# Performance work log

Measured on AMD Instinct MI355X. Metric: run time of the kernel, lower is better.

The kernel has to match this reference:

```python
import jax, jax.numpy as jnp
import numpy as np

N_HEAD = 16
N_KV_HEAD = 4
HEAD_DIM = 128
ROPE_BASE = 10000.0


def _rope_cos_sin(T, offset, dtype):
    # inv_freq: [head_dim//2]
    inv_freq = 1.0 / (ROPE_BASE ** (jnp.arange(0, HEAD_DIM, 2, dtype=jnp.float32) / HEAD_DIM))
    pos = jnp.arange(offset, offset + T, dtype=jnp.float32)
    ang = pos[:, None] * inv_freq[None, :]              # [T, hd/2]
    emb = jnp.concatenate([ang, ang], axis=-1)           # [T, hd]
    return jnp.cos(emb).astype(dtype), jnp.sin(emb).astype(dtype)


def _rotate_half(t):
    half = t.shape[-1] // 2
    return jnp.concatenate([-t[..., half:], t[..., :half]], axis=-1)


def _apply_rope(t, cos, sin):
    # t: [B, h, T, hd]; cos/sin: [T, hd]
    return t * cos[None, None] + _rotate_half(t) * sin[None, None]


def setup_inputs() -> dict:
    key = jax.random.key(0)
    ks = jax.random.split(key, 5)
    B, T, C = 4, 2048, 2048
    scale = 0.02
    return {
        "x": jax.random.normal(ks[0], (B, T, C), dtype=jnp.float32),
        "Wq": jax.random.normal(ks[1], (C, C), dtype=jnp.float32) * scale,
        "Wk": jax.random.normal(ks[2], (N_KV_HEAD * HEAD_DIM, C), dtype=jnp.float32) * scale,
        "Wv": jax.random.normal(ks[3], (N_KV_HEAD * HEAD_DIM, C), dtype=jnp.float32) * scale,
        "Wo": jax.random.normal(ks[4], (C, C), dtype=jnp.float32) * scale,
        "offset": 0,
    }


def reference(x, Wq, Wk, Wv, Wo, offset):
    B, T, C = x.shape
    n_rep = N_HEAD // N_KV_HEAD
    # projections (torch Linear: x @ W.T)
    q = (x @ Wq.T).reshape(B, T, N_HEAD, HEAD_DIM).transpose(0, 2, 1, 3)     # [B,H,T,d]
    k = (x @ Wk.T).reshape(B, T, N_KV_HEAD, HEAD_DIM).transpose(0, 2, 1, 3)  # [B,G,T,d]
    v = (x @ Wv.T).reshape(B, T, N_KV_HEAD, HEAD_DIM).transpose(0, 2, 1, 3)  # [B,G,T,d]
    cos, sin = _rope_cos_sin(T, offset, x.dtype)
    q = _apply_rope(q, cos, sin)
    k = _apply_rope(k, cos, sin)
    # GQA without materializing replicated K/V: group q heads by kv head
    qg = q.reshape(B, N_KV_HEAD, n_rep, T, HEAD_DIM)
    scale = 1.0 / jnp.sqrt(jnp.asarray(HEAD_DIM, dtype=x.dtype))
    scores = jnp.einsum('bgrtd,bgsd->bgrts', qg, k) * scale                  # [B,G,r,T,S]
    causal = jnp.tril(jnp.ones((T, T), dtype=bool))
    scores = jnp.where(causal[None, None, None], scores, jnp.asarray(-jnp.inf, dtype=scores.dtype))
    attn = jax.nn.softmax(scores, axis=-1)
    yg = jnp.einsum('bgrts,bgsd->bgrtd', attn, v)                            # [B,G,r,T,d]
    y = yg.reshape(B, N_HEAD, T, HEAD_DIM).transpose(0, 2, 1, 3).reshape(B, T, C)
    return y @ Wo.T
```

## Files before the change

### kernel.cpp

```cpp
#include <hip/hip_runtime.h>
#include <math.h>

#define BATCH 4
#define SEQ   2048
#define CDIM  2048
#define NH    16
#define NG    4
#define HD    128
#define MTOT  (BATCH*SEQ)
#define KVD   (NG*HD)

typedef __attribute__((ext_vector_type(8))) short     bf16x8;
typedef __attribute__((ext_vector_type(8))) unsigned short u16x8;
typedef __attribute__((ext_vector_type(4))) float     f32x4;
typedef unsigned short ushort_t;

static __device__ __forceinline__ unsigned short f2bf(float f) {
  unsigned u = __float_as_uint(f);
  u += 0x7FFF + ((u >> 16) & 1);
  return (unsigned short)(u >> 16);
}
static __device__ __forceinline__ float bf2f(unsigned short h) {
  return __uint_as_float(((unsigned)h) << 16);
}

#define GLOAD_LDS16(gp, lp)                                                        \
  __builtin_amdgcn_global_load_lds((const __attribute__((address_space(1))) void*)(gp), \
                                   (__attribute__((address_space(3))) void*)(lp),  \
                                   16, 0, 0)

__global__ __launch_bounds__(256) void cvt_f32_bf16(
    const float* __restrict__ s, ushort_t* __restrict__ d, int n8)
{
  int i = blockIdx.x * 256 + threadIdx.x;
  if (i >= n8) return;
  const float4* p = (const float4*)(s + (size_t)i * 8);
  float4 a = p[0], b = p[1];
  u16x8 o;
  o[0] = f2bf(a.x); o[1] = f2bf(a.y); o[2] = f2bf(a.z); o[3] = f2bf(a.w);
  o[4] = f2bf(b.x); o[5] = f2bf(b.y); o[6] = f2bf(b.z); o[7] = f2bf(b.w);
  *(u16x8*)(d + (size_t)i * 8) = o;
}

template<int OUTMODE>
__global__ __launch_bounds__(256) void gemm_bt_bf16(
    const ushort_t* __restrict__ A, const ushort_t* __restrict__ B,
    void* __restrict__ C, int M, int N, int K)
{
  __shared__ ushort_t As[128 * 32];
  __shared__ ushort_t Bs[128 * 32];
  const int tid  = threadIdx.x;
  const int lane = tid & 63, w = tid >> 6;
  const int wm = (w >> 1) * 64, wn = (w & 1) * 64;
  const int bm = blockIdx.x * 128, bn = blockIdx.y * 128;

  f32x4 acc[4][4];
#pragma unroll
  for (int m = 0; m < 4; ++m)
#pragma unroll
    for (int n = 0; n < 4; ++n) acc[m][n] = (f32x4){0.f, 0.f, 0.f, 0.f};

  const int srow = tid >> 2;
  const int scol = (tid & 3) * 8;
  const ushort_t* Ap = A + (size_t)(bm + srow) * K + scol;
  const ushort_t* Bp = B + (size_t)(bn + srow) * K + scol;

  const int fr = lane & 15, fg = lane >> 4;

  for (int k0 = 0; k0 < K; k0 += 32) {
    GLOAD_LDS16(Ap + k0,                  As + tid * 8);
    GLOAD_LDS16(Ap + (size_t)64 * K + k0, As + 2048 + tid * 8);
    GLOAD_LDS16(Bp + k0,                  Bs + tid * 8);
    GLOAD_LDS16(Bp + (size_t)64 * K + k0, Bs + 2048 + tid * 8);
    __syncthreads();

    bf16x8 av[4], bv[4];
#pragma unroll
    for (int m = 0; m < 4; ++m)
      av[m] = *(const bf16x8*)(As + (wm + m * 16 + fr) * 32 + fg * 8);
#pragma unroll
    for (int n = 0; n < 4; ++n)
      bv[n] = *(const bf16x8*)(Bs + (wn + n * 16 + fr) * 32 + fg * 8);
#pragma unroll
    for (int m = 0; m < 4; ++m)
#pragma unroll
      for (int n = 0; n < 4; ++n)
        acc[m][n] = __builtin_amdgcn_mfma_f32_16x16x32_bf16(av[m], bv[n], acc[m][n], 0, 0, 0);
    __syncthreads();
  }

  if constexpr (OUTMODE == 2) {
    __shared__ ushort_t Ct[128 * 144];
#pragma unroll
    for (int m = 0; m < 4; ++m)
#pragma unroll
      for (int n = 0; n < 4; ++n)
#pragma unroll
        for (int r = 0; r < 4; ++r)
          Ct[(wn + n * 16 + fr) * 144 + wm + m * 16 + fg * 4 + r] = f2bf(acc[m][n][r]);
    __syncthreads();
    const int col_l = tid >> 1, part = tid & 1;
    ushort_t* dst = (ushort_t*)C + (size_t)(bn + col_l) * M + bm + part * 64;
#pragma unroll
    for (int j = 0; j < 8; ++j)
      *(bf16x8*)(dst + j * 8) = *(const bf16x8*)(Ct + col_l * 144 + part * 64 + j * 8);
  } else {
#pragma unroll
    for (int m = 0; m < 4; ++m)
#pragma unroll
      for (int n = 0; n < 4; ++n)
#pragma unroll
        for (int r = 0; r < 4; ++r) {
          const int row = bm + wm + m * 16 + fg * 4 + r;
          const int col = bn + wn + n * 16 + fr;
          if (OUTMODE == 1) ((float*)C)[(size_t)row * N + col] = acc[m][n][r];
          else              ((ushort_t*)C)[(size_t)row * N + col] = f2bf(acc[m][n][r]);
        }
  }
}

__global__ __launch_bounds__(256) void rope_bf16(
    ushort_t* __restrict__ qf, ushort_t* __restrict__ kf, const int* __restrict__ off)
{
  const int idx  = blockIdx.x * 256 + threadIdx.x;
  const int qtot = MTOT * NH * (HD / 2);
  const int ktot = MTOT * NG * (HD / 2);
  if (idx >= qtot + ktot) return;

  ushort_t* buf; int row, head, i, cols;
  if (idx < qtot) {
    buf = qf; cols = NH * HD;
    row = idx / (NH * (HD / 2));
    int rem = idx % (NH * (HD / 2));
    head = rem / (HD / 2); i = rem % (HD / 2);
  } else {
    int id2 = idx - qtot;
    buf = kf; cols = NG * HD;
    row = id2 / (NG * (HD / 2));
    int rem = id2 % (NG * (HD / 2));
    head = rem / (HD / 2); i = rem % (HD / 2);
  }
  const int   t   = row % SEQ;
  const float pos = (float)(t + off[0]);
  const float inv = powf(10000.0f, -(float)i * (1.0f / 64.0f));
  const float ang = pos * inv;
  const float c = cosf(ang), s = sinf(ang);

  ushort_t* p = buf + (size_t)row * cols + head * HD + i;
  const float lo = bf2f(p[0]), hi = bf2f(p[64]);
  p[0]  = f2bf(lo * c - hi * s);
  p[64] = f2bf(hi * c + lo * s);
}

#define KPAD 136
#define VPAD 72

__global__ __launch_bounds__(256) void attn_mfma(
    const ushort_t* __restrict__ qf,
    const ushort_t* __restrict__ kf,
    const ushort_t* __restrict__ vT,
    ushort_t* __restrict__ yb)
{
  __shared__ ushort_t Ks[64 * KPAD];
  __shared__ ushort_t Vt[128 * VPAD];
  __shared__ ushort_t Ps[64 * VPAD];

  const int tid  = threadIdx.x;
  const int lane = tid & 63, wq = tid >> 6;
  const int bh = blockIdx.x, b = bh >> 4, h = bh & 15, g = h >> 2;
  const int qb = blockIdx.y * 64;
  const int fr = lane & 15, fg = lane >> 4;

  bf16x8 qv[4];
  {
    const ushort_t* qp = qf + (size_t)(b * SEQ + qb + wq * 16 + fr) * CDIM + h * HD + fg * 8;
#pragma unroll
    for (int ds = 0; ds < 4; ++ds) qv[ds] = *(const bf16x8*)(qp + ds * 32);
  }

  f32x4 o[8];
#pragma unroll
  for (int n = 0; n < 8; ++n) o[n] = (f32x4){0.f, 0.f, 0.f, 0.f};
  float mrow[4] = {-1e30f, -1e30f, -1e30f, -1e30f};
  float lrow[4] = {0.f, 0.f, 0.f, 0.f};

  const float scale = 0.088388347648318447f;
  const int nkv = qb / 64 + 1;

  const ushort_t* vtb0 = vT + (size_t)(g * HD) * MTOT + (size_t)b * SEQ;

  for (int kb = 0; kb < nkv; ++kb) {
    const int s0 = kb * 64;
    __syncthreads();

#pragma unroll
    for (int it = 0; it < 4; ++it) {
      const int f4 = tid + it * 256;
      const int r = f4 >> 4, c8 = (f4 & 15) * 8;
      bf16x8 kx = *(const bf16x8*)(kf + (size_t)(b * SEQ + s0 + r) * KVD + g * HD + c8);
      *(bf16x8*)(Ks + r * KPAD + c8) = kx;
    }
    const ushort_t* vtb = vtb0 + s0;
#pragma unroll
    for (int it = 0; it < 4; ++it) {
      const int gi = tid + it * 256;
      const int d = gi >> 3, gg = gi & 7;
      bf16x8 vx = *(const bf16x8*)(vtb + (size_t)d * MTOT + gg * 8);
      *(bf16x8*)(Vt + d * VPAD + gg * 8) = vx;
    }
    __syncthreads();

    f32x4 st[4];
#pragma unroll
    for (int n = 0; n < 4; ++n) st[n] = (f32x4){0.f, 0.f, 0.f, 0.f};
#pragma unroll
    for (int ds = 0; ds < 4; ++ds) {
#pragma unroll
      for (int n = 0; n < 4; ++n) {
        bf16x8 kv = *(const bf16x8*)(Ks + (n * 16 + fr) * KPAD + ds * 32 + fg * 8);
        st[n] = __builtin_amdgcn_mfma_f32_16x16x32_bf16(qv[ds], kv, st[n], 0, 0, 0);
      }
    }

    float es[4];
#pragma unroll
    for (int r = 0; r < 4; ++r) {
      const int grow = qb + wq * 16 + fg * 4 + r;
      float sv[4], mx = -1e30f;
#pragma unroll
      for (int n = 0; n < 4; ++n) {
        const int col = s0 + n * 16 + fr;
        float v = st[n][r] * scale;
        v = (col <= grow) ? v : -1e30f;
        sv[n] = v; mx = fmaxf(mx, v);
      }
      mx = fmaxf(mx, __shfl_xor(mx, 1, 64));
      mx = fmaxf(mx, __shfl_xor(mx, 2, 64));
      mx = fmaxf(mx, __shfl_xor(mx, 4, 64));
      mx = fmaxf(mx, __shfl_xor(mx, 8, 64));
      const float mnew = fmaxf(mrow[r], mx);
      es[r] = __expf(mrow[r] - mnew);
      float sum = 0.f;
      const int prow = (wq * 16 + fg * 4 + r) * VPAD;
#pragma unroll
      for (int n = 0; n < 4; ++n) {
        const float p = __expf(sv[n] - mnew);
        sum += p;
        Ps[prow + n * 16 + fr] = f2bf(p);
      }
      sum += __shfl_xor(sum, 1, 64);
      sum += __shfl_xor(sum, 2, 64);
      sum += __shfl_xor(sum, 4, 64);
      sum += __shfl_xor(sum, 8, 64);
      lrow[r] = lrow[r] * es[r] + sum;
      mrow[r] = mnew;
    }
#pragma unroll
    for (int n = 0; n < 8; ++n)
#pragma unroll
      for (int r = 0; r < 4; ++r) o[n][r] *= es[r];

#pragma unroll
    for (int ks = 0; ks < 2; ++ks) {
      bf16x8 pa = *(const bf16x8*)(Ps + (wq * 16 + fr) * VPAD + ks * 32 + fg * 8);
#pragma unroll
      for (int n = 0; n < 8; ++n) {
        bf16x8 vb = *(const bf16x8*)(Vt + (n * 16 + fr) * VPAD + ks * 32 + fg * 8);
        o[n] = __builtin_amdgcn_mfma_f32_16x16x32_bf16(pa, vb, o[n], 0, 0, 0);
      }
    }
  }

#pragma unroll
  for (int n = 0; n < 8; ++n)
#pragma unroll
    for (int r = 0; r < 4; ++r) {
      const int row = qb + wq * 16 + fg * 4 + r;
      const int col = h * HD + n * 16 + fr;
      yb[(size_t)(b * SEQ + row) * CDIM + col] = f2bf(o[n][r] / lrow[r]);
    }
}

extern "C" void kernel_launch(void* const* d_in, const int* in_sizes, int n_in,
                              void* d_out, int out_size, void* d_ws, size_t ws_size,
                              hipStream_t stream) {
  const float* x  = (const float*)d_in[0];
  const float* Wq = (const float*)d_in[1];
  const float* Wk = (const float*)d_in[2];
  const float* Wv = (const float*)d_in[3];
  const float* Wo = (const float*)d_in[4];
  const int*   off = (const int*)d_in[5];
  float* out = (float*)d_out;

  ushort_t* xb  = (ushort_t*)d_ws;
  ushort_t* wqb = xb  + (size_t)MTOT * CDIM;
  ushort_t* wkb = wqb + (size_t)CDIM * CDIM;
  ushort_t* wvb = wkb + (size_t)KVD * CDIM;
  ushort_t* wob = wvb + (size_t)KVD * CDIM;
  ushort_t* qb_ = wob + (size_t)CDIM * CDIM;
  ushort_t* kb_ = qb_ + (size_t)MTOT * CDIM;
  ushort_t* vT_ = kb_ + (size_t)MTOT * KVD;
  ushort_t* yb_ = vT_ + (size_t)MTOT * KVD;

  dim3 blk(256);

  int n8;
  n8 = MTOT * CDIM / 8; cvt_f32_bf16<<<(n8 + 255) / 256, blk, 0, stream>>>(x,  xb,  n8);
  n8 = CDIM * CDIM / 8; cvt_f32_bf16<<<(n8 + 255) / 256, blk, 0, stream>>>(Wq, wqb, n8);
  n8 = KVD  * CDIM / 8; cvt_f32_bf16<<<(n8 + 255) / 256, blk, 0, stream>>>(Wk, wkb, n8);
  n8 = KVD  * CDIM / 8; cvt_f32_bf16<<<(n8 + 255) / 256, blk, 0, stream>>>(Wv, wvb, n8);
  n8 = CDIM * CDIM / 8; cvt_f32_bf16<<<(n8 + 255) / 256, blk, 0, stream>>>(Wo, wob, n8);

  gemm_bt_bf16<0><<<dim3(MTOT / 128, CDIM / 128), blk, 0, stream>>>(xb, wqb, qb_, MTOT, CDIM, CDIM);
  gemm_bt_bf16<0><<<dim3(MTOT / 128, KVD / 128),  blk, 0, stream>>>(xb, wkb, kb_, MTOT, KVD, CDIM);
  gemm_bt_bf16<2><<<dim3(MTOT / 128, KVD / 128),  blk, 0, stream>>>(xb, wvb, vT_, MTOT, KVD, CDIM);

  const int total_pairs = MTOT * (NH + NG) * (HD / 2);
  rope_bf16<<<(total_pairs + 255) / 256, blk, 0, stream>>>(qb_, kb_, off);

  attn_mfma<<<dim3(BATCH * NH, SEQ / 64), blk, 0, stream>>>(qb_, kb_, vT_, yb_);

  gemm_bt_bf16<1><<<dim3(MTOT / 128, CDIM / 128), blk, 0, stream>>>(yb_, wob, out, MTOT, CDIM, CDIM);
}
```

Measured before the change: 856.5 us.

## Enlarge attention query tile to 128 rows with register-prefetched KV pipeline

The attention kernel now processes 128 query rows per block, with each wave owning two 16-row MFMA tiles, so every K/V tile staged in shared memory is reused across twice as many queries. The next K/V tile is prefetched into registers during compute and written to LDS after a barrier. The change also skips fully masked tiles per wave, drops mask work on fully unmasked tiles, folds the softmax scale into an exp2 constant, and adds s_setprio around the MFMA sections. The cost is more register pressure (launch bounds now request 2 blocks per SM), half as many blocks in the grid, and an extra barrier per iteration.

After: 720.2 us. 1.19x faster.

```diff
diff --git a/kernel.cpp b/kernel.cpp
--- a/kernel.cpp
+++ b/kernel.cpp
@@ -155,7 +155,7 @@
 #define KPAD 136
 #define VPAD 72
 
-__global__ __launch_bounds__(256) void attn_mfma(
+__global__ __launch_bounds__(256, 2) void attn_mfma(
     const ushort_t* __restrict__ qf,
     const ushort_t* __restrict__ kf,
     const ushort_t* __restrict__ vT,
@@ -163,122 +163,168 @@
 {
   __shared__ ushort_t Ks[64 * KPAD];
   __shared__ ushort_t Vt[128 * VPAD];
-  __shared__ ushort_t Ps[64 * VPAD];
+  __shared__ ushort_t Ps[128 * VPAD];
 
   const int tid  = threadIdx.x;
   const int lane = tid & 63, wq = tid >> 6;
   const int bh = blockIdx.x, b = bh >> 4, h = bh & 15, g = h >> 2;
-  const int qb = blockIdx.y * 64;
+  const int qb = blockIdx.y * 128;
   const int fr = lane & 15, fg = lane >> 4;
-
-  bf16x8 qv[4];
-  {
-    const ushort_t* qp = qf + (size_t)(b * SEQ + qb + wq * 16 + fr) * CDIM + h * HD + fg * 8;
-#pragma unroll
-    for (int ds = 0; ds < 4; ++ds) qv[ds] = *(const bf16x8*)(qp + ds * 32);
-  }
-
-  f32x4 o[8];
-#pragma unroll
-  for (int n = 0; n < 8; ++n) o[n] = (f32x4){0.f, 0.f, 0.f, 0.f};
-  float mrow[4] = {-1e30f, -1e30f, -1e30f, -1e30f};
-  float lrow[4] = {0.f, 0.f, 0.f, 0.f};
-
-  const float scale = 0.088388347648318447f;
-  const int nkv = qb / 64 + 1;
+  const int wrow0 = qb + wq * 32;
+
+  bf16x8 qv[2][4];
+#pragma unroll
+  for (int rb = 0; rb < 2; ++rb) {
+    const ushort_t* qp = qf + (size_t)(b * SEQ + wrow0 + rb * 16 + fr) * CDIM + h * HD + fg * 8;
+#pragma unroll
+    for (int ds = 0; ds < 4; ++ds) qv[rb][ds] = *(const bf16x8*)(qp + ds * 32);
+  }
+
+  f32x4 o[2][8];
+#pragma unroll
+  for (int rb = 0; rb < 2; ++rb)
+#pragma unroll
+    for (int n = 0; n < 8; ++n) o[rb][n] = (f32x4){0.f, 0.f, 0.f, 0.f};
+  float mrow[2][4], lrow[2][4];
+#pragma unroll
+  for (int rb = 0; rb < 2; ++rb)
+#pragma unroll
+    for (int r = 0; r < 4; ++r) { mrow[rb][r] = -1e30f; lrow[rb][r] = 0.f; }
+
+  const float K2 = 0.12751743671f;
+  const int nkv = qb / 64 + 2;
 
   const ushort_t* vtb0 = vT + (size_t)(g * HD) * MTOT + (size_t)b * SEQ;
+  const ushort_t* kfb  = kf + (size_t)(b * SEQ) * KVD + g * HD;
+
+  bf16x8 kpre[4], vpre[4];
+
+  auto prefetch = [&](int s0n) {
+#pragma unroll
+    for (int it = 0; it < 4; ++it) {
+      const int f4 = tid + it * 256;
+      kpre[it] = *(const bf16x8*)(kfb + (size_t)(s0n + (f4 >> 4)) * KVD + (f4 & 15) * 8);
+    }
+#pragma unroll
+    for (int it = 0; it < 4; ++it) {
+      const int f4 = tid + it * 256;
+      vpre[it] = *(const bf16x8*)(vtb0 + s0n + (size_t)(f4 >> 3) * MTOT + (f4 & 7) * 8);
+    }
+  };
+  auto writetile = [&]() {
+#pragma unroll
+    for (int it = 0; it < 4; ++it) {
+      const int f4 = tid + it * 256;
+      *(bf16x8*)(Ks + (f4 >> 4) * KPAD + (f4 & 15) * 8) = kpre[it];
+    }
+#pragma unroll
+    for (int it = 0; it < 4; ++it) {
+      const int f4 = tid + it * 256;
+      *(bf16x8*)(Vt + (f4 >> 3) * VPAD + (f4 & 7) * 8) = vpre[it];
+    }
+  };
+
+  prefetch(0);
+  writetile();
+  __syncthreads();
 
   for (int kb = 0; kb < nkv; ++kb) {
     const int s0 = kb * 64;
-    __syncthreads();
-
-#pragma unroll
-    for (int it = 0; it < 4; ++it) {
-      const int f4 = tid + it * 256;
-      const int r = f4 >> 4, c8 = (f4 & 15) * 8;
-      bf16x8 kx = *(const bf16x8*)(kf + (size_t)(b * SEQ + s0 + r) * KVD + g * HD + c8);
-      *(bf16x8*)(Ks + r * KPAD + c8) = kx;
-    }
-    const ushort_t* vtb = vtb0 + s0;
-#pragma unroll
-    for (int it = 0; it < 4; ++it) {
-      const int gi = tid + it * 256;
-      const int d = gi >> 3, gg = gi & 7;
-      bf16x8 vx = *(const bf16x8*)(vtb + (size_t)d * MTOT + gg * 8);
-      *(bf16x8*)(Vt + d * VPAD + gg * 8) = vx;
-    }
-    __syncthreads();
-
-    f32x4 st[4];
-#pragma unroll
-    for (int n = 0; n < 4; ++n) st[n] = (f32x4){0.f, 0.f, 0.f, 0.f};
-#pragma unroll
-    for (int ds = 0; ds < 4; ++ds) {
-#pragma unroll
-      for (int n = 0; n < 4; ++n) {
-        bf16x8 kv = *(const bf16x8*)(Ks + (n * 16 + fr) * KPAD + ds * 32 + fg * 8);
-        st[n] = __builtin_amdgcn_mfma_f32_16x16x32_bf16(qv[ds], kv, st[n], 0, 0, 0);
+    const bool last = (kb + 1 >= nkv);
+    if (!last) prefetch(s0 + 64);
+
+    if (s0 <= wrow0 + 31) {
+      f32x4 st[2][4];
+#pragma unroll
+      for (int rb = 0; rb < 2; ++rb)
+#pragma unroll
+        for (int n = 0; n < 4; ++n) st[rb][n] = (f32x4){0.f, 0.f, 0.f, 0.f};
+      __builtin_amdgcn_s_setprio(1);
+#pragma unroll
+      for (int ds = 0; ds < 4; ++ds)
+#pragma unroll
+        for (int n = 0; n < 4; ++n) {
+          bf16x8 kvf = *(const bf16x8*)(Ks + (n * 16 + fr) * KPAD + ds * 32 + fg * 8);
+          st[0][n] = __builtin_amdgcn_mfma_f32_16x16x32_bf16(qv[0][ds], kvf, st[0][n], 0, 0, 0);
+          st[1][n] = __builtin_amdgcn_mfma_f32_16x16x32_bf16(qv[1][ds], kvf, st[1][n], 0, 0, 0);
+        }
+      __builtin_amdgcn_s_setprio(0);
+
+      const bool nomask = (s0 + 63 <= wrow0);
+      float es[2][4];
+#pragma unroll
+      for (int rb = 0; rb < 2; ++rb)
+#pragma unroll
+        for (int r = 0; r < 4; ++r) {
+          const int grow = wrow0 + rb * 16 + fg * 4 + r;
+          float sv[4], mx = -1e30f;
+#pragma unroll
+          for (int n = 0; n < 4; ++n) {
+            float v = st[rb][n][r];
+            if (!nomask) {
+              const int col = s0 + n * 16 + fr;
+              v = (col <= grow) ? v : -1e30f;
+            }
+            sv[n] = v; mx = fmaxf(mx, v);
+          }
+          mx = fmaxf(mx, __shfl_xor(mx, 1, 64));
+          mx = fmaxf(mx, __shfl_xor(mx, 2, 64));
+          mx = fmaxf(mx, __shfl_xor(mx, 4, 64));
+          mx = fmaxf(mx, __shfl_xor(mx, 8, 64));
+          const float mnew = fmaxf(mrow[rb][r], mx);
+          es[rb][r] = exp2f((mrow[rb][r] - mnew) * K2);
+          float sum = 0.f;
+          const int prow = (wq * 32 + rb * 16 + fg * 4 + r) * VPAD;
+#pragma unroll
+          for (int n = 0; n < 4; ++n) {
+            const float p = exp2f((sv[n] - mnew) * K2);
+            sum += p;
+            Ps[prow + n * 16 + fr] = f2bf(p);
+          }
+          sum += __shfl_xor(sum, 1, 64);
+          sum += __shfl_xor(sum, 2, 64);
+          sum += __shfl_xor(sum, 4, 64);
+          sum += __shfl_xor(sum, 8, 64);
+          lrow[rb][r] = lrow[rb][r] * es[rb][r] + sum;
+          mrow[rb][r] = mnew;
+        }
+#pragma unroll
+      for (int rb = 0; rb < 2; ++rb)
+#pragma unroll
+        for (int n = 0; n < 8; ++n)
+#pragma unroll
+          for (int r = 0; r < 4; ++r) o[rb][n][r] *= es[rb][r];
+
+      __builtin_amdgcn_s_setprio(1);
+#pragma unroll
+      for (int ks = 0; ks < 2; ++ks) {
+        bf16x8 pa0 = *(const bf16x8*)(Ps + (wq * 32 + fr) * VPAD + ks * 32 + fg * 8);
+        bf16x8 pa1 = *(const bf16x8*)(Ps + (wq * 32 + 16 + fr) * VPAD + ks * 32 + fg * 8);
+#pragma unroll
+        for (int n = 0; n < 8; ++n) {
+          bf16x8 vbf = *(const bf16x8*)(Vt + (n * 16 + fr) * VPAD + ks * 32 + fg * 8);
+          o[0][n] = __builtin_amdgcn_mfma_f32_16x16x32_bf16(pa0, vbf, o[0][n], 0, 0, 0);
+          o[1][n] = __builtin_amdgcn_mfma_f32_16x16x32_bf16(pa1, vbf, o[1][n], 0, 0, 0);
+        }
       }
-    }
-
-    float es[4];
-#pragma unroll
-    for (int r = 0; r < 4; ++r) {
-      const int grow = qb + wq * 16 + fg * 4 + r;
-      float sv[4], mx = -1e30f;
-#pragma unroll
-      for (int n = 0; n < 4; ++n) {
-        const int col = s0 + n * 16 + fr;
-        float v = st[n][r] * scale;
-        v = (col <= grow) ? v : -1e30f;
-        sv[n] = v; mx = fmaxf(mx, v);
+      __builtin_amdgcn_s_setprio(0);
+    }
+
+    __syncthreads();
+    if (!last) writetile();
+    __syncthreads();
+  }
+
+#pragma unroll
+  for (int rb = 0; rb < 2; ++rb)
+#pragma unroll
+    for (int n = 0; n < 8; ++n)
+#pragma unroll
+      for (int r = 0; r < 4; ++r) {
+        const int row = qb + wq * 32 + rb * 16 + fg * 4 + r;
+        const int col = h * HD + n * 16 + fr;
+        yb[(size_t)(b * SEQ + row) * CDIM + col] = f2bf(o[rb][n][r] / lrow[rb][r]);
       }
-      mx = fmaxf(mx, __shfl_xor(mx, 1, 64));
-      mx = fmaxf(mx, __shfl_xor(mx, 2, 64));
-      mx = fmaxf(mx, __shfl_xor(mx, 4, 64));
-      mx = fmaxf(mx, __shfl_xor(mx, 8, 64));
-      const float mnew = fmaxf(mrow[r], mx);
-      es[r] = __expf(mrow[r] - mnew);
-      float sum = 0.f;
-      const int prow = (wq * 16 + fg * 4 + r) * VPAD;
-#pragma unroll
-      for (int n = 0; n < 4; ++n) {
-        const float p = __expf(sv[n] - mnew);
-        sum += p;
-        Ps[prow + n * 16 + fr] = f2bf(p);
-      }
-      sum += __shfl_xor(sum, 1, 64);
-      sum += __shfl_xor(sum, 2, 64);
-      sum += __shfl_xor(sum, 4, 64);
-      sum += __shfl_xor(sum, 8, 64);
-      lrow[r] = lrow[r] * es[r] + sum;
-      mrow[r] = mnew;
-    }
-#pragma unroll
-    for (int n = 0; n < 8; ++n)
-#pragma unroll
-      for (int r = 0; r < 4; ++r) o[n][r] *= es[r];
-
-#pragma unroll
-    for (int ks = 0; ks < 2; ++ks) {
-      bf16x8 pa = *(const bf16x8*)(Ps + (wq * 16 + fr) * VPAD + ks * 32 + fg * 8);
-#pragma unroll
-      for (int n = 0; n < 8; ++n) {
-        bf16x8 vb = *(const bf16x8*)(Vt + (n * 16 + fr) * VPAD + ks * 32 + fg * 8);
-        o[n] = __builtin_amdgcn_mfma_f32_16x16x32_bf16(pa, vb, o[n], 0, 0, 0);
-      }
-    }
-  }
-
-#pragma unroll
-  for (int n = 0; n < 8; ++n)
-#pragma unroll
-    for (int r = 0; r < 4; ++r) {
-      const int row = qb + wq * 16 + fg * 4 + r;
-      const int col = h * HD + n * 16 + fr;
-      yb[(size_t)(b * SEQ + row) * CDIM + col] = f2bf(o[n][r] / lrow[r]);
-    }
 }
 
 extern "C" void kernel_launch(void* const* d_in, const int* in_sizes, int n_in,
@@ -318,7 +364,7 @@
   const int total_pairs = MTOT * (NH + NG) * (HD / 2);
   rope_bf16<<<(total_pairs + 255) / 256, blk, 0, stream>>>(qb_, kb_, off);
 
-  attn_mfma<<<dim3(BATCH * NH, SEQ / 64), blk, 0, stream>>>(qb_, kb_, vT_, yb_);
+  attn_mfma<<<dim3(BATCH * NH, SEQ / 128), blk, 0, stream>>>(qb_, kb_, vT_, yb_);
 
   gemm_bt_bf16<1><<<dim3(MTOT / 128, CDIM / 128), blk, 0, stream>>>(yb_, wob, out, MTOT, CDIM, CDIM);
 }
```
